# Optimization experiments

Hardware: AMD Instinct MI355X
Metric: run time of the kernel (lower is better)

The kernel has to match this reference:

```python
import jax, jax.numpy as jnp
import numpy as np

N, S, H, B = 4096, 128, 768, 128  # hypotheses, seq_len, hidden, utterances
NBEST = N // B


def _seg_softmax(x, seg, num_segments):
    # softmax within each n-best group (segments along last axis of a 1-D vector)
    m = jax.ops.segment_max(x, seg, num_segments=num_segments)
    ex = jnp.exp(x - m[seg])
    s = jax.ops.segment_sum(ex, seg, num_segments=num_segments)
    return ex / s[seg]


def setup_inputs() -> dict:
    key = jax.random.key(0)
    ks = jax.random.split(key, 6)
    pooler_output = jax.random.normal(ks[0], (N, H), jnp.float32)
    last_hidden_state = jax.random.normal(ks[1], (N, S, H), jnp.float32)
    attention_mask = jnp.ones((N, S), jnp.float32)
    am_score = jax.random.normal(ks[2], (N, 1), jnp.float32)
    ctc_score = jax.random.normal(ks[3], (N, 1), jnp.float32)
    # one-hot label: first hypothesis of each n-best group is the oracle
    labels = jnp.zeros((N,), jnp.float32).at[jnp.arange(B) * NBEST].set(1.0)
    W = jax.random.normal(ks[4], (H + 2, 1), jnp.float32) * 0.02
    b = jnp.zeros((1,), jnp.float32)
    nBestIndex = jnp.full((B,), NBEST, jnp.int32)  # group sizes
    return {
        'pooler_output': pooler_output,
        'last_hidden_state': last_hidden_state,
        'attention_mask': attention_mask,
        'am_score': am_score,
        'ctc_score': ctc_score,
        'labels': labels,
        'W': W,
        'b': b,
        'nBestIndex': nBestIndex,
    }


def reference(pooler_output, last_hidden_state, attention_mask, am_score,
              ctc_score, labels, W, b, nBestIndex):
    num_seg = nBestIndex.shape[0]
    n = pooler_output.shape[0]
    seg = jnp.repeat(jnp.arange(num_seg), nBestIndex, total_repeat_length=n)

    # AvgPooling: masked mean over sequence -> [N, H]
    pooled = (last_hidden_state * attention_mask[..., None]).sum(axis=1) \
             / attention_mask.sum(axis=1, keepdims=True)

    # concat pooler with am/ctc scores -> [N, 770], linear -> scalar score per hyp
    concat_state = jnp.concatenate([pooler_output, am_score, ctc_score], axis=-1)
    final_score = (concat_state @ W + b).squeeze(-1)  # [N]

    # segmented (n-best) softmax over scores, then CE loss against one-hot labels
    final_prob = _seg_softmax(final_score, seg, num_seg)
    ce_loss = -jnp.sum(labels * jnp.log(final_prob)) / n

    # similarity matrix between pooler outputs and avg-pooled embeddings [N, N]
    sim = jnp.einsum('id,jd->ij', pooler_output, pooled)
    # per-row segmented softmax (vectorized version of the original Python loop)
    sim_prob = jax.vmap(lambda r: _seg_softmax(r, seg, num_seg))(sim)
    contrast_loss = -jnp.sum(jnp.diagonal(sim_prob)) / num_seg

    loss = ce_loss + contrast_loss
    return final_score, loss
```

## Files before the change

kernel.cpp:

```cpp
#include <hip/hip_runtime.h>
#include <math.h>

typedef float f32x4 __attribute__((ext_vector_type(4)));


__global__ void seg_kernel(const int* __restrict__ nbest,
                           int* __restrict__ starts, int* __restrict__ seg,
                           float* __restrict__ loss, int B) {
    __shared__ int s_starts[1025];
    if (threadIdx.x == 0) {
        int off = 0;
        for (int g = 0; g < B; ++g) { s_starts[g] = off; starts[g] = off; off += nbest[g]; }
        s_starts[B] = off; starts[B] = off;
        *loss = 0.f;
    }
    __syncthreads();
    for (int g = 0; g < B; ++g) {
        const int s0 = s_starts[g], s1 = s_starts[g + 1];
        for (int i = s0 + (int)threadIdx.x; i < s1; i += blockDim.x) seg[i] = g;
    }
}

__global__ void poolscore_kernel(const float* __restrict__ lhs,
                                 const float* __restrict__ mask,
                                 const float* __restrict__ pooler,
                                 const float* __restrict__ am,
                                 const float* __restrict__ ctc,
                                 const float* __restrict__ W,
                                 const float* __restrict__ bb,
                                 float* __restrict__ pooled,
                                 float* __restrict__ score,
                                 int S, int H) {
    __shared__ float smask[1024];
    const int j  = blockIdx.x;
    const int t  = threadIdx.x;
    const int Hv = H >> 2;

    const float* mrow = mask + (size_t)j * S;
    for (int s = t; s < S; s += blockDim.x) smask[s] = mrow[s];
    __syncthreads();

    float msum = 0.f;
    for (int s = 0; s < S; ++s) msum += smask[s];

    const f32x4* row = (const f32x4*)(lhs + (size_t)j * S * H);
    f32x4 acc = {0.f, 0.f, 0.f, 0.f};
#pragma unroll 8
    for (int s = 0; s < S; ++s) {
        f32x4 v = __builtin_nontemporal_load(&row[(size_t)s * Hv + t]);
        acc += v * smask[s];
    }
    const f32x4 o = acc * (1.0f / msum);
    ((f32x4*)(pooled + (size_t)j * H))[t] = o;

    if (t < 64) {
        const f32x4* pr = (const f32x4*)(pooler + (size_t)j * H);
        const f32x4* Wv = (const f32x4*)W;
        float a = 0.f;
        for (int k = t; k < Hv; k += 64) {
            f32x4 p = pr[k] * Wv[k];
            a += p.x + p.y + p.z + p.w;
        }
        for (int d = 32; d > 0; d >>= 1) a += __shfl_xor(a, d, 64);
        if (t == 0)
            score[j] = a + am[j] * W[H] + ctc[j] * W[H + 1] + bb[0];
    }
}

__global__ void finale_kernel(const float* __restrict__ pooler,
                              const float* __restrict__ pooled,
                              const float* __restrict__ score,
                              const float* __restrict__ labels,
                              const int* __restrict__ starts,
                              const int* __restrict__ seg,
                              float* __restrict__ loss,
                              int H, int N, int B) {
    const int bid = blockIdx.x;
    if (bid >= N) {
        const int g = bid - N;
        const int lane = threadIdx.x;
        if (lane >= 64) return;
        const int s0 = starts[g], sz = starts[g + 1] - s0;
        float m = -INFINITY;
        for (int idx = lane; idx < sz; idx += 64) m = fmaxf(m, score[s0 + idx]);
        for (int d = 32; d > 0; d >>= 1) m = fmaxf(m, __shfl_xor(m, d, 64));
        float s = 0.f;
        for (int idx = lane; idx < sz; idx += 64) s += expf(score[s0 + idx] - m);
        for (int d = 32; d > 0; d >>= 1) s += __shfl_xor(s, d, 64);
        const float ls = logf(s);
        float c = 0.f;
        for (int idx = lane; idx < sz; idx += 64) {
            float lb = labels[s0 + idx];
            if (lb != 0.f) c += lb * (score[s0 + idx] - m - ls);
        }
        for (int d = 32; d > 0; d >>= 1) c += __shfl_xor(c, d, 64);
        if (lane == 0) atomicAdd(loss, -c / (float)N);
        return;
    }
    __shared__ float simv[512];
    const int i  = bid;
    const int g  = seg[i];
    const int s0 = starts[g], sz = starts[g + 1] - s0;
    const int wid = threadIdx.x >> 6, lane = threadIdx.x & 63;
    const int nw  = blockDim.x >> 6;
    const int Hv  = H >> 2;
    const f32x4* pi = (const f32x4*)(pooler + (size_t)i * H);
    for (int j = wid; j < sz; j += nw) {
        const f32x4* pj = (const f32x4*)(pooled + (size_t)(s0 + j) * H);
        float acc = 0.f;
        for (int k = lane; k < Hv; k += 64) {
            f32x4 p = pi[k] * pj[k];
            acc += p.x + p.y + p.z + p.w;
        }
        for (int d = 32; d > 0; d >>= 1) acc += __shfl_xor(acc, d, 64);
        if (lane == 0) simv[j] = acc;
    }
    __syncthreads();
    if (wid == 0) {
        float m = -INFINITY;
        for (int idx = lane; idx < sz; idx += 64) m = fmaxf(m, simv[idx]);
        for (int d = 32; d > 0; d >>= 1) m = fmaxf(m, __shfl_xor(m, d, 64));
        float s = 0.f;
        for (int idx = lane; idx < sz; idx += 64) s += expf(simv[idx] - m);
        for (int d = 32; d > 0; d >>= 1) s += __shfl_xor(s, d, 64);
        if (lane == 0) {
            const int p = i - s0;
            const float prob = expf(simv[p] - m) / s;
            atomicAdd(loss, -prob / (float)B);
        }
    }
}

extern "C" void kernel_launch(void* const* d_in, const int* in_sizes, int n_in,
                              void* d_out, int out_size, void* d_ws, size_t ws_size,
                              hipStream_t stream) {
    const float* pooler = (const float*)d_in[0];
    const float* lhs    = (const float*)d_in[1];
    const float* mask   = (const float*)d_in[2];
    const float* am     = (const float*)d_in[3];
    const float* ctc    = (const float*)d_in[4];
    const float* labels = (const float*)d_in[5];
    const float* W      = (const float*)d_in[6];
    const float* bb     = (const float*)d_in[7];
    const int*   nbest  = (const int*)d_in[8];

    const int N = in_sizes[5];
    const int B = in_sizes[8];
    const int H = in_sizes[0] / N;
    const int S = in_sizes[2] / N;

    float* out  = (float*)d_out;
    float* loss = out + N;

    float* pooled = (float*)d_ws;
    int*   starts = (int*)((char*)d_ws + (size_t)N * H * sizeof(float));
    int*   seg    = starts + (B + 1);

    hipLaunchKernelGGL(seg_kernel, dim3(1), dim3(256), 0, stream,
                       nbest, starts, seg, loss, B);
    hipLaunchKernelGGL(poolscore_kernel, dim3(N), dim3(H / 4), 0, stream,
                       lhs, mask, pooler, am, ctc, W, bb, pooled, out, S, H);
    hipLaunchKernelGGL(finale_kernel, dim3(N + B), dim3(256), 0, stream,
                       pooler, pooled, out, labels, starts, seg, loss, H, N, B);
}
```

Baseline: 356.9 us.

## Assign one wavefront per hypothesis row in pooling and parallelize segment setup

The pooling kernel now maps one 64-lane wavefront to each hypothesis instead of one 192-thread block. Each lane streams three float4 columns per sequence step, which gives more loads in flight per thread and removes the shared-memory mask staging and its barrier. The mask is read directly per step and summed in the same loop. The segment setup kernel now loads group sizes into shared memory and fills seg with one thread per group rather than a serial per-group block loop. This adds an H-specialized path with a generic fallback, and the unchanged finale kernel remains the other main cost.

Result: faster. 327.6 us (-8.2%).

```diff
diff --git a/kernel.cpp b/kernel.cpp
--- a/kernel.cpp
+++ b/kernel.cpp
@@ -7,52 +7,100 @@
 __global__ void seg_kernel(const int* __restrict__ nbest,
                            int* __restrict__ starts, int* __restrict__ seg,
                            float* __restrict__ loss, int B) {
-    __shared__ int s_starts[1025];
-    if (threadIdx.x == 0) {
+    __shared__ int sh[1025];
+    const int t = threadIdx.x;
+    for (int g = t; g < B; g += blockDim.x) sh[g] = nbest[g];
+    __syncthreads();
+    if (t == 0) {
         int off = 0;
-        for (int g = 0; g < B; ++g) { s_starts[g] = off; starts[g] = off; off += nbest[g]; }
-        s_starts[B] = off; starts[B] = off;
+        for (int g = 0; g < B; ++g) { int v = sh[g]; sh[g] = off; off += v; }
+        sh[B] = off;
         *loss = 0.f;
     }
     __syncthreads();
-    for (int g = 0; g < B; ++g) {
-        const int s0 = s_starts[g], s1 = s_starts[g + 1];
-        for (int i = s0 + (int)threadIdx.x; i < s1; i += blockDim.x) seg[i] = g;
-    }
-}
-
-__global__ void poolscore_kernel(const float* __restrict__ lhs,
-                                 const float* __restrict__ mask,
-                                 const float* __restrict__ pooler,
-                                 const float* __restrict__ am,
-                                 const float* __restrict__ ctc,
-                                 const float* __restrict__ W,
-                                 const float* __restrict__ bb,
-                                 float* __restrict__ pooled,
-                                 float* __restrict__ score,
-                                 int S, int H) {
-    __shared__ float smask[1024];
+    for (int g = t; g <= B; g += blockDim.x) starts[g] = sh[g];
+    for (int g = t; g < B; g += blockDim.x) {
+        const int s0 = sh[g], s1 = sh[g + 1];
+        for (int i = s0; i < s1; ++i) seg[i] = g;
+    }
+}
+
+__global__ __launch_bounds__(256, 4)
+void pool_kernel_h768(const float* __restrict__ lhs,
+                      const float* __restrict__ mask,
+                      const float* __restrict__ pooler,
+                      const float* __restrict__ am,
+                      const float* __restrict__ ctc,
+                      const float* __restrict__ W,
+                      const float* __restrict__ bb,
+                      float* __restrict__ pooled,
+                      float* __restrict__ score,
+                      int N, int S) {
+    const int H  = 768;
+    const int Hv = 192;
+    const int wid  = threadIdx.x >> 6;
+    const int lane = threadIdx.x & 63;
+    const int j = blockIdx.x * 4 + wid;
+    if (j >= N) return;
+
+    const f32x4* row  = (const f32x4*)(lhs + (size_t)j * S * H) + lane;
+    const float* mrow = mask + (size_t)j * S;
+
+    f32x4 a0 = {0.f,0.f,0.f,0.f}, a1 = a0, a2 = a0;
+    float msum = 0.f;
+#pragma unroll 8
+    for (int s = 0; s < S; ++s) {
+        float m = mrow[s];
+        const f32x4* p = row + (size_t)s * Hv;
+        f32x4 v0 = __builtin_nontemporal_load(p);
+        f32x4 v1 = __builtin_nontemporal_load(p + 64);
+        f32x4 v2 = __builtin_nontemporal_load(p + 128);
+        a0 += v0 * m; a1 += v1 * m; a2 += v2 * m;
+        msum += m;
+    }
+    const float inv = 1.0f / msum;
+    f32x4* prow = (f32x4*)(pooled + (size_t)j * H);
+    prow[lane]       = a0 * inv;
+    prow[lane + 64]  = a1 * inv;
+    prow[lane + 128] = a2 * inv;
+
+    const f32x4* pr = (const f32x4*)(pooler + (size_t)j * H);
+    const f32x4* Wv = (const f32x4*)W;
+    float acc = 0.f;
+#pragma unroll
+    for (int k = lane; k < Hv; k += 64) {
+        f32x4 p = pr[k] * Wv[k];
+        acc += p.x + p.y + p.z + p.w;
+    }
+    for (int d = 32; d > 0; d >>= 1) acc += __shfl_xor(acc, d, 64);
+    if (lane == 0)
+        score[j] = acc + am[j] * W[H] + ctc[j] * W[H + 1] + bb[0];
+}
+
+__global__ void pool_kernel_generic(const float* __restrict__ lhs,
+                                    const float* __restrict__ mask,
+                                    const float* __restrict__ pooler,
+                                    const float* __restrict__ am,
+                                    const float* __restrict__ ctc,
+                                    const float* __restrict__ W,
+                                    const float* __restrict__ bb,
+                                    float* __restrict__ pooled,
+                                    float* __restrict__ score,
+                                    int S, int H) {
     const int j  = blockIdx.x;
     const int t  = threadIdx.x;
     const int Hv = H >> 2;
-
+    const f32x4* row  = (const f32x4*)(lhs + (size_t)j * S * H);
     const float* mrow = mask + (size_t)j * S;
-    for (int s = t; s < S; s += blockDim.x) smask[s] = mrow[s];
-    __syncthreads();
-
+    f32x4 acc = {0.f,0.f,0.f,0.f};
     float msum = 0.f;
-    for (int s = 0; s < S; ++s) msum += smask[s];
-
-    const f32x4* row = (const f32x4*)(lhs + (size_t)j * S * H);
-    f32x4 acc = {0.f, 0.f, 0.f, 0.f};
-#pragma unroll 8
+#pragma unroll 4
     for (int s = 0; s < S; ++s) {
-        f32x4 v = __builtin_nontemporal_load(&row[(size_t)s * Hv + t]);
-        acc += v * smask[s];
-    }
-    const f32x4 o = acc * (1.0f / msum);
-    ((f32x4*)(pooled + (size_t)j * H))[t] = o;
-
+        float m = mrow[s];
+        acc += __builtin_nontemporal_load(&row[(size_t)s * Hv + t]) * m;
+        msum += m;
+    }
+    ((f32x4*)(pooled + (size_t)j * H))[t] = acc * (1.0f / msum);
     if (t < 64) {
         const f32x4* pr = (const f32x4*)(pooler + (size_t)j * H);
         const f32x4* Wv = (const f32x4*)W;
@@ -158,8 +206,15 @@
 
     hipLaunchKernelGGL(seg_kernel, dim3(1), dim3(256), 0, stream,
                        nbest, starts, seg, loss, B);
-    hipLaunchKernelGGL(poolscore_kernel, dim3(N), dim3(H / 4), 0, stream,
-                       lhs, mask, pooler, am, ctc, W, bb, pooled, out, S, H);
+    if (H == 768) {
+        hipLaunchKernelGGL(pool_kernel_h768, dim3((N + 3) / 4), dim3(256), 0,
+                           stream, lhs, mask, pooler, am, ctc, W, bb,
+                           pooled, out, N, S);
+    } else {
+        hipLaunchKernelGGL(pool_kernel_generic, dim3(N), dim3(H / 4), 0,
+                           stream, lhs, mask, pooler, am, ctc, W, bb,
+                           pooled, out, S, H);
+    }
     hipLaunchKernelGGL(finale_kernel, dim3(N + B), dim3(256), 0, stream,
                        pooler, pooled, out, labels, starts, seg, loss, H, N, B);
 }
```
